# Performance work log

Hardware: AMD Instinct MI355X
Metric: run time of the kernel (lower is better)

The kernel has to match this reference:

```python
import jax, jax.numpy as jnp
import numpy as np
from functools import partial

B, N, NCLS = 16, 25200, 80
M_TGT = 50
MAX_DET = 300
CONF_THRES = 0.8
NMS_THRES = 0.4


def cxcywh_to_xyxy(boxes):
    # cxcywh -> xywh -> xyxy (as in tensor_to_dict: cxcywh_to_xywh then xywh_to_xyxy)
    cx, cy, w, h = boxes[..., 0], boxes[..., 1], boxes[..., 2], boxes[..., 3]
    x1 = cx - 0.5 * w
    y1 = cy - 0.5 * h
    return jnp.stack([x1, y1, x1 + w, y1 + h], axis=-1)


def pairwise_iou(b):
    # b: [K,4] xyxy
    x1 = jnp.maximum(b[:, None, 0], b[None, :, 0])
    y1 = jnp.maximum(b[:, None, 1], b[None, :, 1])
    x2 = jnp.minimum(b[:, None, 2], b[None, :, 2])
    y2 = jnp.minimum(b[:, None, 3], b[None, :, 3])
    inter = jnp.clip(x2 - x1, 0.0) * jnp.clip(y2 - y1, 0.0)
    area = jnp.clip(b[:, 2] - b[:, 0], 0.0) * jnp.clip(b[:, 3] - b[:, 1], 0.0)
    return inter / (area[:, None] + area[None, :] - inter + 1e-9)


def nms_one(boxes_xyxy, labels, valid):
    # boxes sorted by score descending; class-aware greedy NMS, fixed K iterations
    K = boxes_xyxy.shape[0]
    iou = pairwise_iou(boxes_xyxy)
    same = labels[:, None] == labels[None, :]
    supp = (iou > NMS_THRES) & same
    idx = jnp.arange(K)

    def body(i, keep):
        kill = supp[i] & (idx > i) & keep[i]
        return keep & ~kill

    return jax.lax.fori_loop(0, K, body, valid)


def post_process(preds):
    # preds: [B, N, 5+C] (cx,cy,w,h,obj,cls...)
    obj = preds[..., 4]
    cls_prob = preds[..., 5:]
    cls_conf = jnp.max(cls_prob, axis=-1)
    cls_id = jnp.argmax(cls_prob, axis=-1)
    score = obj * cls_conf                      # [B,N]
    score = jnp.where(score > CONF_THRES, score, 0.0)
    top_s, top_i = jax.lax.top_k(score, MAX_DET)            # [B,K]
    boxes = jnp.take_along_axis(preds[..., :4], top_i[..., None], axis=1)  # cxcywh [B,K,4]
    labels = jnp.take_along_axis(cls_id, top_i, axis=1)     # [B,K]
    valid = top_s > 0.0
    boxes_xyxy = cxcywh_to_xyxy(boxes)
    keep = jax.vmap(nms_one)(boxes_xyxy, labels, valid)     # [B,K]
    scores = jnp.where(keep, top_s, 0.0)
    boxes_xyxy = jnp.where(keep[..., None], boxes_xyxy, 0.0)
    labels = jnp.where(keep, labels, -1)
    return boxes_xyxy, scores, labels, keep


def process_targets(tt, lengths):
    # tt: [B, M, 6] = cxcywh, score, label ; lengths: [B]
    valid = jnp.arange(tt.shape[1])[None, :] < lengths[:, None]  # [B,M]
    boxes = cxcywh_to_xyxy(tt[..., :4])
    scores = tt[..., 4]
    labels = tt[..., 5].astype(jnp.int32)
    boxes = jnp.where(valid[..., None], boxes, 0.0)
    scores = jnp.where(valid, scores, 0.0)
    labels = jnp.where(valid, labels, -1)
    return boxes, scores, labels, valid


def setup_inputs() -> dict:
    key = jax.random.key(0)
    k1, k2, k3, k4 = jax.random.split(key, 4)
    preds = jax.random.uniform(k1, (B, N, 5 + NCLS), dtype=jnp.float32)
    tgt_boxes = jax.random.uniform(k2, (B, M_TGT, 4), dtype=jnp.float32) * 640.0
    tgt_scores = jnp.ones((B, M_TGT, 1), dtype=jnp.float32)
    tgt_labels = jax.random.randint(k3, (B, M_TGT, 1), 0, NCLS).astype(jnp.float32)
    target_target = jnp.concatenate([tgt_boxes, tgt_scores, tgt_labels], axis=-1)
    target_lengths = jax.random.randint(k4, (B,), 1, M_TGT + 1).astype(jnp.int32)
    return {"preds": preds, "target_target": target_target, "target_lengths": target_lengths}


def reference(preds, target_target, target_lengths):
    pb, ps, pl, pv = post_process(preds)
    tb, ts, tl, tv = process_targets(target_target, target_lengths)
    # @torch.no_grad in original forward
    out = (pb, ps, pl, pv, tb, ts, tl, tv)
    return jax.tree_util.tree_map(jax.lax.stop_gradient, out)
```

## Files before the change

### kernel.cpp

```cpp
#include <hip/hip_runtime.h>
#include <cstdint>

#define BB 16
#define NN 25200
#define NCLS 80
#define NF (5 + NCLS)
#define MAXDET 300
#define MTGT 50
#define CONF 0.8f
#define NMSTH 0.4f
#define WORDS 10
#define NBINS 2048
#define CAPALL 8192
#define SBUF 2048
#define APB 64
#define CPB 394
#define SLOTK 48
#define SCORE_BLOCKS (BB * CPB)
#define NTGT_BLOCKS ((BB * MTGT + 127) / 128)
#define HSTRIDE 33

#define WS_CNTS 0
#define WS_KEYS 32768

#define O_PB 0
#define O_PS (BB * MAXDET * 4)
#define O_PL (O_PS + BB * MAXDET)
#define O_PV (O_PL + BB * MAXDET)
#define O_TB (O_PV + BB * MAXDET)
#define O_TS (O_TB + BB * MTGT * 4)
#define O_TL (O_TS + BB * MTGT)
#define O_TV (O_TL + BB * MTGT)

__global__ __launch_bounds__(128) void k_score(const float* __restrict__ preds,
                                               int* __restrict__ cnts,
                                               unsigned long long* __restrict__ keys,
                                               const float* __restrict__ tt,
                                               const int* __restrict__ len,
                                               float* __restrict__ out) {
    __shared__ float st[APB * NF];
    __shared__ int wbase0;
    int tid = threadIdx.x;
    int bid = blockIdx.x;

    if (bid >= SCORE_BLOCKS) {
        int t = (bid - SCORE_BLOCKS) * 128 + tid;
        if (t < BB * MTGT) {
            int b = t / MTGT, m = t - b * MTGT;
            const float* row = tt + (size_t)t * 6;
            bool valid = m < len[b];
            float cx = row[0], cy = row[1], w = row[2], h = row[3];
            float x1 = cx - 0.5f * w, y1 = cy - 0.5f * h;
            float* tb = out + O_TB + (size_t)t * 4;
            tb[0] = valid ? x1 : 0.f;
            tb[1] = valid ? y1 : 0.f;
            tb[2] = valid ? (x1 + w) : 0.f;
            tb[3] = valid ? (y1 + h) : 0.f;
            out[O_TS + t] = valid ? row[4] : 0.f;
            out[O_TL + t] = valid ? (float)(int)row[5] : -1.f;
            out[O_TV + t] = valid ? 1.f : 0.f;
        }
        return;
    }

    int b  = bid / CPB;
    int cb = bid - b * CPB;
    int count = (cb == CPB - 1) ? (NN - (CPB - 1) * APB) : APB;
    int nv4 = count * NF / 4;

    int w = tid >> 6;
    int lane = tid & 63;
    const float4* src = (const float4*)(preds + ((size_t)b * NN + (size_t)cb * APB) * NF);
    #pragma unroll
    for (int i = 0; i < 11; ++i) {
        int idx = i * 128 + tid;
        if (idx < nv4) {
            __builtin_amdgcn_global_load_lds(
                (const __attribute__((address_space(1))) void*)(src + idx),
                (__attribute__((address_space(3))) void*)(st + (i * 128 + w * 64) * 4),
                16, 0, 0);
        }
    }
    __syncthreads();

    int a = tid >> 1, h = tid & 1;
    const float* cls = st + a * NF + 5 + h * 40;
    float m0 = cls[0], m1 = cls[1], m2 = cls[2], m3 = cls[3];
    #pragma unroll
    for (int f = 4; f < 40; f += 4) {
        m0 = fmaxf(m0, cls[f]);     m1 = fmaxf(m1, cls[f + 1]);
        m2 = fmaxf(m2, cls[f + 2]); m3 = fmaxf(m3, cls[f + 3]);
    }
    float m = fmaxf(fmaxf(m0, m1), fmaxf(m2, m3));
    m = fmaxf(m, __shfl_xor(m, 1));
    float s = st[a * NF + 4] * m;

    bool pass = (h == 0) && (a < count) && (s > CONF);
    unsigned long long mask = __ballot(pass);
    int wcnt = __popcll(mask);
    if (w == 0 && lane == 0) wbase0 = wcnt;
    __syncthreads();
    int base = (w == 0) ? 0 : wbase0;
    if (pass) {
        int pos = base + __popcll(mask & ((1ull << lane) - 1ull));
        if (pos < SLOTK) {
            unsigned u = __float_as_uint(s);
            keys[(size_t)bid * SLOTK + pos] =
                ((unsigned long long)u << 32) |
                (unsigned long long)(0xFFFFFFFFu - (unsigned)(cb * APB + a));
        }
    }
    if (w == 1 && lane == 0) {
        int tot = base + wcnt;
        cnts[bid] = tot < SLOTK ? tot : SLOTK;
    }
}

__global__ __launch_bounds__(1024) void k_post(const int* __restrict__ cnts,
                                               const unsigned long long* __restrict__ keys,
                                               const float* __restrict__ preds,
                                               float* __restrict__ out) {
    __shared__ unsigned long long skall[CAPALL];
    __shared__ unsigned long long sk[SBUF];
    __shared__ unsigned long long skTop[MAXDET];
    __shared__ int hist[64 * HSTRIDE];
    __shared__ float4   sbox[MAXDET];
    __shared__ int      slabel[MAXDET];
    __shared__ float    sscore[MAXDET];
    __shared__ unsigned supp[MAXDET * WORDS];
    __shared__ int wsum[16];
    __shared__ int lcnt, lcnt2, scut;
    int b = blockIdx.x;
    int tid = threadIdx.x;
    int lane = tid & 63;
    int wv = tid >> 6;

    if (tid == 0) { lcnt = 0; lcnt2 = 0; }
    for (int i = tid; i < 64 * HSTRIDE; i += 1024) hist[i] = 0;
    if (tid < MAXDET) skTop[tid] = 0ull;
    __syncthreads();

    int c = (tid < CPB) ? cnts[b * CPB + tid] : 0;
    int inc = c;
    #pragma unroll
    for (int d = 1; d < 64; d <<= 1) {
        int o = __shfl_up(inc, d);
        if (lane >= d) inc += o;
    }
    if (lane == 63) wsum[wv] = inc;
    __syncthreads();
    int wbase = 0;
    #pragma unroll
    for (int q = 0; q < 16; ++q) wbase += (q < wv) ? wsum[q] : 0;
    int base = wbase + inc - c;
    if (tid == 1023) lcnt = wbase + inc;
    if (tid < CPB) {
        const unsigned long long* slot = keys + (size_t)(b * CPB + tid) * SLOTK;
        for (int k = 0; k < c; ++k) {
            int p = base + k;
            if (p < CAPALL) skall[p] = slot[k];
        }
    }
    __syncthreads();
    int M = lcnt; if (M > CAPALL) M = CAPALL;
    for (int i = tid; i < M; i += 1024) {
        unsigned u = (unsigned)(skall[i] >> 32);
        int bin = (int)((u - 0x3F400000u) >> 12);
        bin = bin < 0 ? 0 : (bin > NBINS - 1 ? NBINS - 1 : bin);
        atomicAdd(&hist[(bin >> 5) * HSTRIDE + (bin & 31)], 1);
    }
    __syncthreads();

    if (tid < 64) {
        int sb = 0;
        #pragma unroll
        for (int k = 0; k < 32; ++k) sb += hist[lane * HSTRIDE + k];
        int cum = sb;
        #pragma unroll
        for (int d = 1; d < 64; d <<= 1) {
            int o = __shfl_down(cum, d);
            if (lane + d < 64) cum += o;
        }
        unsigned long long m = __ballot(cum >= MAXDET);
        int cutbin = 0;
        if (m) {
            int cutS = 63 - __clzll(m);
            int tail = (cutS < 63) ? __shfl(cum, cutS + 1) : 0;
            int hh = (lane < 32) ? hist[cutS * HSTRIDE + lane] : 0;
            int c2 = hh;
            #pragma unroll
            for (int d = 1; d < 32; d <<= 1) {
                int o = __shfl_down(c2, d);
                if (lane + d < 32) c2 += o;
            }
            c2 += tail;
            unsigned long long m2 = __ballot(lane < 32 && c2 >= MAXDET);
            int cutL = 63 - __clzll(m2);
            cutbin = cutS * 32 + cutL;
        }
        if (lane == 0) scut = cutbin;
    }
    __syncthreads();
    int cutbin = scut;

    for (int i = tid; i < ((M + 1023) & ~1023); i += 1024) {
        bool pass = false;
        unsigned long long key = 0ull;
        if (i < M) {
            key = skall[i];
            unsigned u = (unsigned)(key >> 32);
            int bin = (int)((u - 0x3F400000u) >> 12);
            bin = bin < 0 ? 0 : (bin > NBINS - 1 ? NBINS - 1 : bin);
            pass = bin >= cutbin;
        }
        unsigned long long mask = __ballot(pass);
        int wcnt = __popcll(mask);
        int bs = 0;
        if (lane == 0 && wcnt) bs = atomicAdd(&lcnt2, wcnt);
        bs = __shfl(bs, 0);
        if (pass) {
            int pos = bs + __popcll(mask & ((1ull << lane) - 1ull));
            if (pos < SBUF) sk[pos] = key;
        }
    }
    __syncthreads();

    int M2 = lcnt2; if (M2 > SBUF) M2 = SBUF;
    for (int c2 = tid; c2 < M2; c2 += 1024) {
        unsigned long long key = sk[c2];
        int rank = 0;
        for (int j = 0; j < M2; ++j) rank += (sk[j] > key) ? 1 : 0;
        if (rank < MAXDET) skTop[rank] = key;
    }
    __syncthreads();

    {
        int k = tid >> 1, h = tid & 1;
        if (k < MAXDET) {
            unsigned long long key = skTop[k];
            unsigned sbits = (unsigned)(key >> 32);
            if (sbits) {
                int idx = (int)(0xFFFFFFFFu - (unsigned)(key & 0xFFFFFFFFu));
                const float* row = preds + ((size_t)b * NN + (size_t)idx) * NF;
                const float* cls = row + 5 + h * 40;
                float v = cls[0]; int ci = h * 40;
                #pragma unroll
                for (int f = 1; f < 40; ++f) {
                    float x = cls[f];
                    if (x > v) { v = x; ci = h * 40 + f; }
                }
                float ov = __shfl_xor(v, 1);
                int   oi = __shfl_xor(ci, 1);
                if (ov > v || (ov == v && oi < ci)) { v = ov; ci = oi; }
                if (h == 0) {
                    float cx = row[0], cy = row[1], w = row[2], hh = row[3];
                    float x1 = cx - 0.5f * w, y1 = cy - 0.5f * hh;
                    float4 bx = { x1, y1, x1 + w, y1 + hh };
                    sbox[k] = bx;
                    slabel[k] = ci;
                    sscore[k] = __uint_as_float(sbits);
                }
            } else if (h == 0) {
                float4 zz = { 0.f, 0.f, 0.f, 0.f };
                sbox[k] = zz; slabel[k] = -1; sscore[k] = 0.f;
            }
        }
    }
    __syncthreads();

    for (int T = tid; T < MAXDET * WORDS; T += 1024) {
        int i  = T / WORDS;
        int jw = T - i * WORDS;
        unsigned word = 0;
        int jbase = jw * 32;
        if (jbase + 31 > i) {
            float4 bi = sbox[i];
            int   li = slabel[i];
            float si = sscore[i];
            float ai = __fmul_rn(fmaxf(__fsub_rn(bi.z, bi.x), 0.f),
                                 fmaxf(__fsub_rn(bi.w, bi.y), 0.f));
            for (int uu = 0; uu < 32; ++uu) {
                int t = (uu + jw) & 31;
                int j = jbase + t;
                if (j > i && j < MAXDET) {
                    if (slabel[j] == li && si > 0.f && sscore[j] > 0.f) {
                        float4 bj = sbox[j];
                        float xx1 = fmaxf(bi.x, bj.x);
                        float yy1 = fmaxf(bi.y, bj.y);
                        float xx2 = fminf(bi.z, bj.z);
                        float yy2 = fminf(bi.w, bj.w);
                        float iw = fmaxf(__fsub_rn(xx2, xx1), 0.f);
                        float ih = fmaxf(__fsub_rn(yy2, yy1), 0.f);
                        float inter = __fmul_rn(iw, ih);
                        float aj = __fmul_rn(fmaxf(__fsub_rn(bj.z, bj.x), 0.f),
                                             fmaxf(__fsub_rn(bj.w, bj.y), 0.f));
                        float den = __fadd_rn(__fsub_rn(__fadd_rn(ai, aj), inter), 1e-9f);
                        float iou = inter / den;
                        if (iou > NMSTH) word |= 1u << t;
                    }
                }
            }
        }
        supp[T] = word;
    }
    __syncthreads();

    if (tid < 64) {
        unsigned keep = 0, nzm = 0;
        #pragma unroll
        for (int s = 0; s < 5; ++s) {
            int k = s * 64 + lane;
            bool kb = (k < MAXDET) && (sscore[k] > 0.f);
            unsigned long long m = __ballot(kb);
            if (lane == 2 * s)     keep = (unsigned)m;
            if (lane == 2 * s + 1) keep = (unsigned)(m >> 32);
            unsigned nz = 0;
            if (k < MAXDET) {
                #pragma unroll
                for (int w = 0; w < WORDS; ++w) nz |= supp[k * WORDS + w];
            }
            unsigned long long mn = __ballot(nz != 0u);
            if (lane == 2 * s)     nzm = (unsigned)mn;
            if (lane == 2 * s + 1) nzm = (unsigned)(mn >> 32);
        }

        for (int i = 0; i < MAXDET; ++i) {
            int idx = i >> 5;
            unsigned kw = __shfl(keep, idx);
            unsigned nw = __shfl(nzm, idx);
            if (((kw & nw) >> (i & 31)) & 1u) {
                if (lane < WORDS) keep &= ~supp[i * WORDS + lane];
            }
        }

        #pragma unroll
        for (int s = 0; s < 5; ++s) {
            int k = s * 64 + lane;
            if (k < MAXDET) {
                unsigned kw = __shfl(keep, k >> 5);
                bool kp = (kw >> (k & 31)) & 1u;
                int g = b * MAXDET + k;
                float4 bx = sbox[k];
                float4 zz = { 0.f, 0.f, 0.f, 0.f };
                ((float4*)(out + O_PB))[g] = kp ? bx : zz;
                out[O_PS + g] = kp ? sscore[k] : 0.f;
                out[O_PL + g] = kp ? (float)slabel[k] : -1.f;
                out[O_PV + g] = kp ? 1.f : 0.f;
            }
        }
    }
}

extern "C" void kernel_launch(void* const* d_in, const int* in_sizes, int n_in,
                              void* d_out, int out_size, void* d_ws, size_t ws_size,
                              hipStream_t stream) {
    const float* preds = (const float*)d_in[0];
    const float* tt    = (const float*)d_in[1];
    const int*   len   = (const int*)d_in[2];
    float* out = (float*)d_out;

    char* ws = (char*)d_ws;
    int* cnts = (int*)(ws + WS_CNTS);
    unsigned long long* keys = (unsigned long long*)(ws + WS_KEYS);

    k_score<<<SCORE_BLOCKS + NTGT_BLOCKS, 128, 0, stream>>>(preds, cnts, keys, tt, len, out);
    k_post <<<BB, 1024, 0, stream>>>(cnts, keys, preds, out);
}
```

Before: 78.91 us.

## Compute argmax and box in score pass, stash per-candidate payload for post kernel

The score kernel now tracks the argmax class index alongside the max, and for each passing candidate writes its xyxy box and label to workspace buffers. The sort key packs a slot index instead of the raw anchor index. The post kernel then gathers its box and label from these compact buffers rather than re-reading and re-scanning 85-float prediction rows from global memory. The cost of this is extra index-tracking compares in the score pass and extra global writes per candidate. It also relies on the packed key preserving the same tie-break order.

```diff
diff --git a/kernel.cpp b/kernel.cpp
--- a/kernel.cpp
+++ b/kernel.cpp
@@ -22,6 +22,8 @@
 
 #define WS_CNTS 0
 #define WS_KEYS 32768
+#define WS_GBOX (WS_KEYS + (size_t)SCORE_BLOCKS * SLOTK * 8)
+#define WS_GLAB (WS_GBOX + (size_t)SCORE_BLOCKS * SLOTK * 16)
 
 #define O_PB 0
 #define O_PS (BB * MAXDET * 4)
@@ -35,6 +37,8 @@
 __global__ __launch_bounds__(128) void k_score(const float* __restrict__ preds,
                                                int* __restrict__ cnts,
                                                unsigned long long* __restrict__ keys,
+                                               float* __restrict__ gbox,
+                                               int* __restrict__ glabel,
                                                const float* __restrict__ tt,
                                                const int* __restrict__ len,
                                                float* __restrict__ out) {
@@ -84,16 +88,26 @@
     __syncthreads();
 
     int a = tid >> 1, h = tid & 1;
-    const float* cls = st + a * NF + 5 + h * 40;
-    float m0 = cls[0], m1 = cls[1], m2 = cls[2], m3 = cls[3];
+    const float* row = st + a * NF;
+    const float* cls = row + 5 + h * 40;
+    float v0 = cls[0], v1 = cls[1], v2 = cls[2], v3 = cls[3];
+    int   i0 = 0,      i1 = 1,      i2 = 2,      i3 = 3;
     #pragma unroll
     for (int f = 4; f < 40; f += 4) {
-        m0 = fmaxf(m0, cls[f]);     m1 = fmaxf(m1, cls[f + 1]);
-        m2 = fmaxf(m2, cls[f + 2]); m3 = fmaxf(m3, cls[f + 3]);
-    }
-    float m = fmaxf(fmaxf(m0, m1), fmaxf(m2, m3));
-    m = fmaxf(m, __shfl_xor(m, 1));
-    float s = st[a * NF + 4] * m;
+        if (cls[f]     > v0) { v0 = cls[f];     i0 = f; }
+        if (cls[f + 1] > v1) { v1 = cls[f + 1]; i1 = f + 1; }
+        if (cls[f + 2] > v2) { v2 = cls[f + 2]; i2 = f + 2; }
+        if (cls[f + 3] > v3) { v3 = cls[f + 3]; i3 = f + 3; }
+    }
+    float v = v0; int ia = i0;
+    if (v1 > v || (v1 == v && i1 < ia)) { v = v1; ia = i1; }
+    if (v2 > v || (v2 == v && i2 < ia)) { v = v2; ia = i2; }
+    if (v3 > v || (v3 == v && i3 < ia)) { v = v3; ia = i3; }
+    int ci = h * 40 + ia;
+    float ov = __shfl_xor(v, 1);
+    int   oi = __shfl_xor(ci, 1);
+    if (ov > v || (ov == v && oi < ci)) { v = ov; ci = oi; }
+    float s = row[4] * v;
 
     bool pass = (h == 0) && (a < count) && (s > CONF);
     unsigned long long mask = __ballot(pass);
@@ -105,9 +119,16 @@
         int pos = base + __popcll(mask & ((1ull << lane) - 1ull));
         if (pos < SLOTK) {
             unsigned u = __float_as_uint(s);
-            keys[(size_t)bid * SLOTK + pos] =
-                ((unsigned long long)u << 32) |
-                (unsigned long long)(0xFFFFFFFFu - (unsigned)(cb * APB + a));
+            unsigned inv = (unsigned)(NN - 1 - (cb * APB + a));
+            unsigned slot = (unsigned)(cb * SLOTK + pos);
+            size_t g = (size_t)bid * SLOTK + pos;
+            keys[g] = ((unsigned long long)u << 32) |
+                      (unsigned long long)((inv << 17) | slot);
+            float cx = row[0], cy = row[1], ww = row[2], hh = row[3];
+            float x1 = cx - 0.5f * ww, y1 = cy - 0.5f * hh;
+            float4 bx = { x1, y1, x1 + ww, y1 + hh };
+            ((float4*)gbox)[g] = bx;
+            glabel[g] = ci;
         }
     }
     if (w == 1 && lane == 0) {
@@ -118,7 +139,8 @@
 
 __global__ __launch_bounds__(1024) void k_post(const int* __restrict__ cnts,
                                                const unsigned long long* __restrict__ keys,
-                                               const float* __restrict__ preds,
+                                               const float* __restrict__ gbox,
+                                               const int* __restrict__ glabel,
                                                float* __restrict__ out) {
     __shared__ unsigned long long skall[CAPALL];
     __shared__ unsigned long long sk[SBUF];
@@ -234,36 +256,17 @@
     }
     __syncthreads();
 
-    {
-        int k = tid >> 1, h = tid & 1;
-        if (k < MAXDET) {
-            unsigned long long key = skTop[k];
-            unsigned sbits = (unsigned)(key >> 32);
-            if (sbits) {
-                int idx = (int)(0xFFFFFFFFu - (unsigned)(key & 0xFFFFFFFFu));
-                const float* row = preds + ((size_t)b * NN + (size_t)idx) * NF;
-                const float* cls = row + 5 + h * 40;
-                float v = cls[0]; int ci = h * 40;
-                #pragma unroll
-                for (int f = 1; f < 40; ++f) {
-                    float x = cls[f];
-                    if (x > v) { v = x; ci = h * 40 + f; }
-                }
-                float ov = __shfl_xor(v, 1);
-                int   oi = __shfl_xor(ci, 1);
-                if (ov > v || (ov == v && oi < ci)) { v = ov; ci = oi; }
-                if (h == 0) {
-                    float cx = row[0], cy = row[1], w = row[2], hh = row[3];
-                    float x1 = cx - 0.5f * w, y1 = cy - 0.5f * hh;
-                    float4 bx = { x1, y1, x1 + w, y1 + hh };
-                    sbox[k] = bx;
-                    slabel[k] = ci;
-                    sscore[k] = __uint_as_float(sbits);
-                }
-            } else if (h == 0) {
-                float4 zz = { 0.f, 0.f, 0.f, 0.f };
-                sbox[k] = zz; slabel[k] = -1; sscore[k] = 0.f;
-            }
+    if (tid < MAXDET) {
+        unsigned long long key = skTop[tid];
+        unsigned sbits = (unsigned)(key >> 32);
+        if (sbits) {
+            size_t g = (size_t)b * (CPB * SLOTK) + (size_t)(key & 0x1FFFFull);
+            sbox[tid]   = ((const float4*)gbox)[g];
+            slabel[tid] = glabel[g];
+            sscore[tid] = __uint_as_float(sbits);
+        } else {
+            float4 zz = { 0.f, 0.f, 0.f, 0.f };
+            sbox[tid] = zz; slabel[tid] = -1; sscore[tid] = 0.f;
         }
     }
     __syncthreads();
@@ -362,7 +365,9 @@
     char* ws = (char*)d_ws;
     int* cnts = (int*)(ws + WS_CNTS);
     unsigned long long* keys = (unsigned long long*)(ws + WS_KEYS);
-
-    k_score<<<SCORE_BLOCKS + NTGT_BLOCKS, 128, 0, stream>>>(preds, cnts, keys, tt, len, out);
-    k_post <<<BB, 1024, 0, stream>>>(cnts, keys, preds, out);
+    float* gbox = (float*)(ws + WS_GBOX);
+    int* glabel = (int*)(ws + WS_GLAB);
+
+    k_score<<<SCORE_BLOCKS + NTGT_BLOCKS, 128, 0, stream>>>(preds, cnts, keys, gbox, glabel, tt, len, out);
+    k_post <<<BB, 1024, 0, stream>>>(cnts, keys, gbox, glabel, out);
 }
```

Result: no change. 78.27 us (-0.8%).
